# Optimization experiments

Hardware: AMD Instinct MI355X
Metric: run time of the kernel (lower is better)

Reference implementation:

```python
import jax, jax.numpy as jnp
import numpy as np

MARGIN = 0.5  # hardcoded in the torch __init__ regardless of the margin arg
P_IDS, K_PER_ID, K_PER_MOD = 32, 8, 4
B, C = P_IDS * K_PER_ID, 1024


def setup_inputs() -> dict:
    key = jax.random.key(0)
    inputs = jax.random.normal(key, (B, C), dtype=jnp.float32)
    # Standard cross-modal ReID sampler: P identities, K instances each,
    # first K/2 from modality 0, last K/2 from modality 1. This guarantees the
    # boolean-mask reshape in the original code is well-formed (M per row).
    targets = jnp.repeat(jnp.arange(P_IDS, dtype=jnp.int32), K_PER_ID)
    subs = jnp.tile(jnp.repeat(jnp.arange(2, dtype=jnp.int32), K_PER_MOD), P_IDS)
    return {"inputs": inputs, "targets": targets, "subs": subs, "m_count": K_PER_MOD}


def _loss(inputs, targets, subs, m_count):
    b, c = inputs.shape
    # Mask construction uses detached inputs in the original (clone().detach()).
    xs = jax.lax.stop_gradient(inputs)
    diff = jnp.abs(xs[:, None, :] - xs[None, :, :])                     # (B,B,C)
    identity_mask = targets[:, None] == targets[None, :]                # (B,B)
    modality_mask = subs[:, None] == subs[None, :]                      # (B,B)
    combined = identity_mask & modality_mask                            # (B,B)

    # diff[combined].reshape(B, M, C): every row has exactly m_count trues;
    # stable argsort recovers the selected column indices in ascending order,
    # matching torch's row-major boolean-mask gather.
    order = jnp.argsort(jnp.where(combined, 0, 1), axis=1)              # stable
    idx = order[:, :m_count]                                            # (B,M)
    modality_diff = jnp.take_along_axis(diff, idx[:, :, None], axis=1)  # (B,M,C)

    mean_md = modality_diff.mean(-1, keepdims=True)                     # (B,M,1)
    m_counts = (modality_diff < mean_md * MARGIN).sum(1)                # (B,C) int
    # mdm[i,j,c] = m_counts[i,c] * m_counts[j,c]  (detached float mask)
    mdm = (m_counts[:, None, :] * m_counts[None, :, :]).astype(inputs.dtype)  # (B,B,C)

    mean_d = diff.mean(-1, keepdims=True)                               # (B,B,1)
    idm = (diff < mean_d * MARGIN).astype(inputs.dtype)                 # (B,B,C)

    # Gradient-carrying pairwise differences (vectorized form of the B-loop).
    d = inputs[:, None, :] - inputs[None, :, :]                         # (B,B,C)
    mod_dist = jnp.sqrt(jnp.maximum(((d * mdm) ** 2).sum(-1), 1e-12))   # (B,B)
    id_dist = jnp.sqrt(jnp.maximum(((d * idm) ** 2).sum(-1), 1e-12))    # (B,B)
    id_dist = jnp.where(identity_mask, jnp.inf, id_dist)                # drop same-id

    per_row = jnp.maximum(mod_dist.max(axis=1) * 10.0 - id_dist.min(axis=1), 0.0)
    return per_row.mean()


def reference(inputs, targets, subs, m_count):
    return _loss(inputs, targets, subs, m_count)
```

## Files before the change

kernel.cpp:

```cpp
#include <hip/hip_runtime.h>
#include <math.h>

#define BB 256
#define CC 1024
#define CC4 (CC/4)
#define MARGIN 0.5f
#define NTILE 32
#define JPT 8

__global__ __launch_bounds__(64) void mcsq_kernel(
    const float* __restrict__ x, const int* __restrict__ targets,
    const int* __restrict__ subs, const int* __restrict__ m_count_p,
    float* __restrict__ mcsq)
{
    const int i = blockIdx.x;
    const int lane = threadIdx.x;
    const int ti = targets[i], si = subs[i];
    int mc = *m_count_p;
    if (mc > 8) mc = 8;

    unsigned long long masks[4];
    #pragma unroll
    for (int q = 0; q < 4; ++q) {
        const int j = q * 64 + lane;
        masks[q] = __ballot(targets[j] == ti && subs[j] == si);
    }
    int idx[8];
    int cnt = 0;
    for (int q = 0; q < 4 && cnt < mc; ++q) {
        unsigned long long m = masks[q];
        while (m && cnt < mc) {
            const int b = __ffsll(m) - 1;
            idx[cnt++] = q * 64 + b;
            m &= m - 1;
        }
    }
    for (int q = 0; q < 4 && cnt < mc; ++q) {
        unsigned long long m = ~masks[q];
        while (m && cnt < mc) {
            const int b = __ffsll(m) - 1;
            idx[cnt++] = q * 64 + b;
            m &= m - 1;
        }
    }

    const float4* x4 = (const float4*)x;
    float4 xi[4];
    #pragma unroll
    for (int t = 0; t < 4; ++t) xi[t] = x4[(long)i * CC4 + lane + 64 * t];

    float4 c4[4];
    #pragma unroll
    for (int t = 0; t < 4; ++t) c4[t] = make_float4(0.f, 0.f, 0.f, 0.f);

    for (int k = 0; k < cnt; ++k) {
        float4 ad[4];
        float s = 0.f;
        #pragma unroll
        for (int t = 0; t < 4; ++t) {
            const float4 xj = x4[(long)idx[k] * CC4 + lane + 64 * t];
            ad[t].x = fabsf(xi[t].x - xj.x);
            ad[t].y = fabsf(xi[t].y - xj.y);
            ad[t].z = fabsf(xi[t].z - xj.z);
            ad[t].w = fabsf(xi[t].w - xj.w);
            s += ad[t].x + ad[t].y + ad[t].z + ad[t].w;
        }
        #pragma unroll
        for (int off = 32; off > 0; off >>= 1) s += __shfl_xor(s, off, 64);
        const float thr = s * (MARGIN / CC);
        #pragma unroll
        for (int t = 0; t < 4; ++t) {
            c4[t].x += (ad[t].x < thr) ? 1.f : 0.f;
            c4[t].y += (ad[t].y < thr) ? 1.f : 0.f;
            c4[t].z += (ad[t].z < thr) ? 1.f : 0.f;
            c4[t].w += (ad[t].w < thr) ? 1.f : 0.f;
        }
    }
    float4* m4 = (float4*)mcsq;
    #pragma unroll
    for (int t = 0; t < 4; ++t) {
        float4 o;
        o.x = c4[t].x * c4[t].x;
        o.y = c4[t].y * c4[t].y;
        o.z = c4[t].z * c4[t].z;
        o.w = c4[t].w * c4[t].w;
        m4[(long)i * CC4 + lane + 64 * t] = o;
    }
}

__global__ __launch_bounds__(256) void pair_kernel(
    const float* __restrict__ x, const float* __restrict__ mcsq,
    const int* __restrict__ targets,
    float* __restrict__ pmax, float* __restrict__ pmin)
{
    const int tid  = threadIdx.x;
    const int lane = tid & 63;
    const int gw   = blockIdx.x * 4 + (tid >> 6);
    const int p    = gw >> 5;
    const int jt   = gw & 31;
    const int i0 = 2 * p, i1 = 2 * p + 1;

    const float4* x4 = (const float4*)x;
    const float4* m4 = (const float4*)mcsq;

    float4 xi0[4], xi1[4], mi0[4], mi1[4];
    #pragma unroll
    for (int t = 0; t < 4; ++t) {
        const int c4 = lane + 64 * t;
        xi0[t] = x4[(long)i0 * CC4 + c4];
        xi1[t] = x4[(long)i1 * CC4 + c4];
        mi0[t] = m4[(long)i0 * CC4 + c4];
        mi1[t] = m4[(long)i1 * CC4 + c4];
    }
    const int t0 = targets[i0], t1 = targets[i1];

    float max0 = 0.f, max1 = 0.f;
    float min0 = INFINITY, min1 = INFINITY;

    for (int jj = 0; jj < JPT; ++jj) {
        const int j = jt * JPT + jj;
        float4 xa[4], ma[4];
        float s0 = 0.f, s1 = 0.f;
        #pragma unroll
        for (int t = 0; t < 4; ++t) {
            const int c4 = lane + 64 * t;
            xa[t] = x4[(long)j * CC4 + c4];
            ma[t] = m4[(long)j * CC4 + c4];
            s0 += fabsf(xi0[t].x - xa[t].x) + fabsf(xi0[t].y - xa[t].y)
                + fabsf(xi0[t].z - xa[t].z) + fabsf(xi0[t].w - xa[t].w);
            s1 += fabsf(xi1[t].x - xa[t].x) + fabsf(xi1[t].y - xa[t].y)
                + fabsf(xi1[t].z - xa[t].z) + fabsf(xi1[t].w - xa[t].w);
        }
        #pragma unroll
        for (int off = 32; off > 0; off >>= 1) {
            s0 += __shfl_xor(s0, off, 64);
            s1 += __shfl_xor(s1, off, 64);
        }
        const float thr0 = s0 * (MARGIN / CC);
        const float thr1 = s1 * (MARGIN / CC);

        float ids0 = 0.f, ids1 = 0.f, md0 = 0.f, md1 = 0.f;
        #pragma unroll
        for (int t = 0; t < 4; ++t) {
            #pragma unroll
            for (int u = 0; u < 4; ++u) {
                const float xav = (&xa[t].x)[u];
                const float mav = (&ma[t].x)[u];
                const float d0 = (&xi0[t].x)[u] - xav;
                const float q0 = d0 * d0;
                ids0 += (fabsf(d0) < thr0) ? q0 : 0.f;
                md0  += q0 * (&mi0[t].x)[u] * mav;
                const float d1 = (&xi1[t].x)[u] - xav;
                const float q1 = d1 * d1;
                ids1 += (fabsf(d1) < thr1) ? q1 : 0.f;
                md1  += q1 * (&mi1[t].x)[u] * mav;
            }
        }
        #pragma unroll
        for (int off = 32; off > 0; off >>= 1) {
            ids0 += __shfl_xor(ids0, off, 64);
            ids1 += __shfl_xor(ids1, off, 64);
            md0  += __shfl_xor(md0,  off, 64);
            md1  += __shfl_xor(md1,  off, 64);
        }
        max0 = fmaxf(max0, sqrtf(fmaxf(md0, 1e-12f)));
        max1 = fmaxf(max1, sqrtf(fmaxf(md1, 1e-12f)));
        const int tj = targets[j];
        if (tj != t0) min0 = fminf(min0, sqrtf(fmaxf(ids0, 1e-12f)));
        if (tj != t1) min1 = fminf(min1, sqrtf(fmaxf(ids1, 1e-12f)));
    }
    if (lane == 0) {
        pmax[i0 * NTILE + jt] = max0;
        pmax[i1 * NTILE + jt] = max1;
        pmin[i0 * NTILE + jt] = min0;
        pmin[i1 * NTILE + jt] = min1;
    }
}

__global__ __launch_bounds__(256) void final_kernel(
    const float* __restrict__ pmax, const float* __restrict__ pmin,
    float* __restrict__ out)
{
    const int i = threadIdx.x;
    float mx = 0.f, mn = INFINITY;
    for (int t = 0; t < NTILE; ++t) {
        mx = fmaxf(mx, pmax[i * NTILE + t]);
        mn = fminf(mn, pmin[i * NTILE + t]);
    }
    float per = fmaxf(mx * 10.f - mn, 0.f);
    __shared__ float red[256];
    red[i] = per;
    __syncthreads();
    for (int off = 128; off > 0; off >>= 1) {
        if (i < off) red[i] += red[i + off];
        __syncthreads();
    }
    if (i == 0) out[0] = red[0] * (1.0f / BB);
}

extern "C" void kernel_launch(void* const* d_in, const int* in_sizes, int n_in,
                              void* d_out, int out_size, void* d_ws, size_t ws_size,
                              hipStream_t stream)
{
    const float* x       = (const float*)d_in[0];
    const int*   targets = (const int*)d_in[1];
    const int*   subs    = (const int*)d_in[2];
    const int*   m_count = (const int*)d_in[3];
    float* out  = (float*)d_out;

    float* mcsq = (float*)d_ws;
    float* pmax = mcsq + (long)BB * CC;
    float* pmin = pmax + BB * NTILE;

    mcsq_kernel <<<BB,   64, 0, stream>>>(x, targets, subs, m_count, mcsq);
    pair_kernel <<<1024, 256, 0, stream>>>(x, mcsq, targets, pmax, pmin);
    final_kernel<<<1,   256, 0, stream>>>(pmax, pmin, out);
}
```

Before: 96.42 us.

## Exploit pairwise symmetry to compute only upper-triangular pair tiles

The pair kernel now walks only the upper triangle of (row-pair, column-tile) work items, mapped with a closed-form triangular index, so each symmetric pair distance is computed once. Each computed value is also written to transposed partial buffers, and the final kernel merges the row-wise and transposed partials to recover every row's max and min. This roughly halves the pairwise distance arithmetic and memory traffic. In exchange it adds extra partial stores, more complex index math, and a longer serial reduction in the single-block final kernel.

New measurement: 117.9 us. +22.3%, slower.

```diff
diff --git a/kernel.cpp b/kernel.cpp
--- a/kernel.cpp
+++ b/kernel.cpp
@@ -5,8 +5,9 @@
 #define CC 1024
 #define CC4 (CC/4)
 #define MARGIN 0.5f
-#define NTILE 32
-#define JPT 8
+#define NTILE 64
+#define JPT 4
+#define NP  128
 
 __global__ __launch_bounds__(64) void mcsq_kernel(
     const float* __restrict__ x, const int* __restrict__ targets,
@@ -91,13 +92,23 @@
 __global__ __launch_bounds__(256) void pair_kernel(
     const float* __restrict__ x, const float* __restrict__ mcsq,
     const int* __restrict__ targets,
-    float* __restrict__ pmax, float* __restrict__ pmin)
+    float* __restrict__ pmax, float* __restrict__ pmin,
+    float* __restrict__ pmaxT, float* __restrict__ pminT)
 {
     const int tid  = threadIdx.x;
     const int lane = tid & 63;
     const int gw   = blockIdx.x * 4 + (tid >> 6);
-    const int p    = gw >> 5;
-    const int jt   = gw & 31;
+
+    int h = (int)((129.0f - sqrtf(16641.0f - 4.0f * (float)gw)) * 0.5f);
+    if (h > 63) h = 63;
+    if (h < 0) h = 0;
+    while (h > 0 && (129 * h - h * h) > gw) --h;
+    while ((129 * (h + 1) - (h + 1) * (h + 1)) <= gw) ++h;
+    const int r     = gw - (129 * h - h * h);
+    const int cnt_h = 64 - h;
+    const int p     = 2 * h + r / cnt_h;
+    const int jt    = h + r % cnt_h;
+
     const int i0 = 2 * p, i1 = 2 * p + 1;
 
     const float4* x4 = (const float4*)x;
@@ -163,11 +174,19 @@
             md0  += __shfl_xor(md0,  off, 64);
             md1  += __shfl_xor(md1,  off, 64);
         }
-        max0 = fmaxf(max0, sqrtf(fmaxf(md0, 1e-12f)));
-        max1 = fmaxf(max1, sqrtf(fmaxf(md1, 1e-12f)));
+        const float mod0 = sqrtf(fmaxf(md0, 1e-12f));
+        const float mod1 = sqrtf(fmaxf(md1, 1e-12f));
+        max0 = fmaxf(max0, mod0);
+        max1 = fmaxf(max1, mod1);
+        float id0 = sqrtf(fmaxf(ids0, 1e-12f));
+        float id1 = sqrtf(fmaxf(ids1, 1e-12f));
         const int tj = targets[j];
-        if (tj != t0) min0 = fminf(min0, sqrtf(fmaxf(ids0, 1e-12f)));
-        if (tj != t1) min1 = fminf(min1, sqrtf(fmaxf(ids1, 1e-12f)));
+        if (tj != t0) min0 = fminf(min0, id0); else id0 = INFINITY;
+        if (tj != t1) min1 = fminf(min1, id1); else id1 = INFINITY;
+        if (lane == 0) {
+            pmaxT[j * NP + p] = fmaxf(mod0, mod1);
+            pminT[j * NP + p] = fminf(id0, id1);
+        }
     }
     if (lane == 0) {
         pmax[i0 * NTILE + jt] = max0;
@@ -179,13 +198,20 @@
 
 __global__ __launch_bounds__(256) void final_kernel(
     const float* __restrict__ pmax, const float* __restrict__ pmin,
+    const float* __restrict__ pmaxT, const float* __restrict__ pminT,
     float* __restrict__ out)
 {
     const int i = threadIdx.x;
+    const int s = i >> 2;
     float mx = 0.f, mn = INFINITY;
-    for (int t = 0; t < NTILE; ++t) {
+    for (int t = s; t < NTILE; ++t) {
         mx = fmaxf(mx, pmax[i * NTILE + t]);
         mn = fminf(mn, pmin[i * NTILE + t]);
+    }
+    const int pv = 2 * s + 2;
+    for (int p = 0; p < pv; ++p) {
+        mx = fmaxf(mx, pmaxT[i * NP + p]);
+        mn = fminf(mn, pminT[i * NP + p]);
     }
     float per = fmaxf(mx * 10.f - mn, 0.f);
     __shared__ float red[256];
@@ -208,11 +234,13 @@
     const int*   m_count = (const int*)d_in[3];
     float* out  = (float*)d_out;
 
-    float* mcsq = (float*)d_ws;
-    float* pmax = mcsq + (long)BB * CC;
-    float* pmin = pmax + BB * NTILE;
+    float* mcsq  = (float*)d_ws;
+    float* pmax  = mcsq  + (long)BB * CC;
+    float* pmin  = pmax  + BB * NTILE;
+    float* pmaxT = pmin  + BB * NTILE;
+    float* pminT = pmaxT + BB * NP;
 
     mcsq_kernel <<<BB,   64, 0, stream>>>(x, targets, subs, m_count, mcsq);
-    pair_kernel <<<1024, 256, 0, stream>>>(x, mcsq, targets, pmax, pmin);
-    final_kernel<<<1,   256, 0, stream>>>(pmax, pmin, out);
-}
+    pair_kernel <<<1040, 256, 0, stream>>>(x, mcsq, targets, pmax, pmin, pmaxT, pminT);
+    final_kernel<<<1,   256, 0, stream>>>(pmax, pmin, pmaxT, pminT, out);
+}
```

## Restructure pairwise pass into LDS-tiled two-pass kernels with channel-split atomics

Applied to the files above, without the earlier changes.

Replaces the per-wave pair kernel, which re-read full rows of x and mcsq from global memory for every pair, with two shared-memory-tiled kernels. The first accumulates L1 distances for 32x32 row blocks. The second computes masked squared distances, with each thread handling a 2x2 pair register tile over a channel slice and reducing across slices with global atomicAdd. Workspace zeroing is folded into mcsq_kernel. The final reduction is spread over 256 blocks that finish with an atomic counter and a last-block write. This trades global reloads and shuffle reductions for LDS reuse, but adds an extra pass, many float atomics and order-dependent summation.

Result: slower. 99.80 us (+3.5%).

```diff
diff --git a/kernel.cpp b/kernel.cpp
--- a/kernel.cpp
+++ b/kernel.cpp
@@ -5,16 +5,22 @@
 #define CC 1024
 #define CC4 (CC/4)
 #define MARGIN 0.5f
-#define NTILE 32
-#define JPT 8
+
 
 __global__ __launch_bounds__(64) void mcsq_kernel(
     const float* __restrict__ x, const int* __restrict__ targets,
     const int* __restrict__ subs, const int* __restrict__ m_count_p,
-    float* __restrict__ mcsq)
+    float* __restrict__ mcsq, float* __restrict__ zbase,
+    float* __restrict__ acc, unsigned int* __restrict__ cnt_g)
 {
     const int i = blockIdx.x;
     const int lane = threadIdx.x;
+    if (i == 0 && lane == 0) { *acc = 0.f; *cnt_g = 0u; }
+    {
+        const int g = i * 64 + lane;
+        #pragma unroll
+        for (int t = 0; t < 12; ++t) zbase[g + 16384 * t] = 0.f;
+    }
     const int ti = targets[i], si = subs[i];
     int mc = *m_count_p;
     if (mc > 8) mc = 8;
@@ -88,114 +94,154 @@
     }
 }
 
-__global__ __launch_bounds__(256) void pair_kernel(
+__global__ __launch_bounds__(256) void pass1_kernel(
+    const float* __restrict__ x, float* __restrict__ S)
+{
+    __shared__ float xs[64 * 129];
+    const int b  = blockIdx.x;
+    const int cc = b & 7;
+    const int jt = (b >> 3) & 7;
+    const int it = b >> 6;
+    const int l  = threadIdx.x;
+
+    const float4* x4 = (const float4*)x;
+    #pragma unroll
+    for (int k = 0; k < 8; ++k) {
+        const int idx = l + 256 * k;
+        const int row = idx >> 5;
+        const int c4  = idx & 31;
+        const int grow = (row < 32) ? (it * 32 + row) : (jt * 32 + row - 32);
+        const float4 v = x4[grow * CC4 + cc * 32 + c4];
+        float* dst = &xs[row * 129 + c4 * 4];
+        dst[0] = v.x; dst[1] = v.y; dst[2] = v.z; dst[3] = v.w;
+    }
+    __syncthreads();
+
+    const int li = l >> 4, lj = l & 15;
+    const float* pi0 = &xs[(2 * li) * 129];
+    const float* pi1 = &xs[(2 * li + 1) * 129];
+    const float* pj0 = &xs[(32 + 2 * lj) * 129];
+    const float* pj1 = &xs[(32 + 2 * lj + 1) * 129];
+    float s00 = 0.f, s01 = 0.f, s10 = 0.f, s11 = 0.f;
+    #pragma unroll 8
+    for (int c = 0; c < 128; ++c) {
+        const float a0 = pi0[c], a1 = pi1[c], b0 = pj0[c], b1 = pj1[c];
+        s00 += fabsf(a0 - b0); s01 += fabsf(a0 - b1);
+        s10 += fabsf(a1 - b0); s11 += fabsf(a1 - b1);
+    }
+    const int gi0 = it * 32 + 2 * li, gj0 = jt * 32 + 2 * lj;
+    atomicAdd(&S[gi0 * BB + gj0],           s00);
+    atomicAdd(&S[gi0 * BB + gj0 + 1],       s01);
+    atomicAdd(&S[(gi0 + 1) * BB + gj0],     s10);
+    atomicAdd(&S[(gi0 + 1) * BB + gj0 + 1], s11);
+}
+
+__global__ __launch_bounds__(256) void pass2_kernel(
     const float* __restrict__ x, const float* __restrict__ mcsq,
-    const int* __restrict__ targets,
-    float* __restrict__ pmax, float* __restrict__ pmin)
-{
-    const int tid  = threadIdx.x;
-    const int lane = tid & 63;
-    const int gw   = blockIdx.x * 4 + (tid >> 6);
-    const int p    = gw >> 5;
-    const int jt   = gw & 31;
-    const int i0 = 2 * p, i1 = 2 * p + 1;
+    const float* __restrict__ S,
+    float* __restrict__ IDS, float* __restrict__ MD)
+{
+    __shared__ float xs[64 * 65];
+    __shared__ float ms[64 * 65];
+    const int b  = blockIdx.x;
+    const int cc = b & 15;
+    const int jt = (b >> 4) & 7;
+    const int it = b >> 7;
+    const int l  = threadIdx.x;
 
     const float4* x4 = (const float4*)x;
     const float4* m4 = (const float4*)mcsq;
-
-    float4 xi0[4], xi1[4], mi0[4], mi1[4];
-    #pragma unroll
-    for (int t = 0; t < 4; ++t) {
-        const int c4 = lane + 64 * t;
-        xi0[t] = x4[(long)i0 * CC4 + c4];
-        xi1[t] = x4[(long)i1 * CC4 + c4];
-        mi0[t] = m4[(long)i0 * CC4 + c4];
-        mi1[t] = m4[(long)i1 * CC4 + c4];
-    }
-    const int t0 = targets[i0], t1 = targets[i1];
-
-    float max0 = 0.f, max1 = 0.f;
-    float min0 = INFINITY, min1 = INFINITY;
-
-    for (int jj = 0; jj < JPT; ++jj) {
-        const int j = jt * JPT + jj;
-        float4 xa[4], ma[4];
-        float s0 = 0.f, s1 = 0.f;
-        #pragma unroll
-        for (int t = 0; t < 4; ++t) {
-            const int c4 = lane + 64 * t;
-            xa[t] = x4[(long)j * CC4 + c4];
-            ma[t] = m4[(long)j * CC4 + c4];
-            s0 += fabsf(xi0[t].x - xa[t].x) + fabsf(xi0[t].y - xa[t].y)
-                + fabsf(xi0[t].z - xa[t].z) + fabsf(xi0[t].w - xa[t].w);
-            s1 += fabsf(xi1[t].x - xa[t].x) + fabsf(xi1[t].y - xa[t].y)
-                + fabsf(xi1[t].z - xa[t].z) + fabsf(xi1[t].w - xa[t].w);
-        }
-        #pragma unroll
-        for (int off = 32; off > 0; off >>= 1) {
-            s0 += __shfl_xor(s0, off, 64);
-            s1 += __shfl_xor(s1, off, 64);
-        }
-        const float thr0 = s0 * (MARGIN / CC);
-        const float thr1 = s1 * (MARGIN / CC);
-
-        float ids0 = 0.f, ids1 = 0.f, md0 = 0.f, md1 = 0.f;
-        #pragma unroll
-        for (int t = 0; t < 4; ++t) {
-            #pragma unroll
-            for (int u = 0; u < 4; ++u) {
-                const float xav = (&xa[t].x)[u];
-                const float mav = (&ma[t].x)[u];
-                const float d0 = (&xi0[t].x)[u] - xav;
-                const float q0 = d0 * d0;
-                ids0 += (fabsf(d0) < thr0) ? q0 : 0.f;
-                md0  += q0 * (&mi0[t].x)[u] * mav;
-                const float d1 = (&xi1[t].x)[u] - xav;
-                const float q1 = d1 * d1;
-                ids1 += (fabsf(d1) < thr1) ? q1 : 0.f;
-                md1  += q1 * (&mi1[t].x)[u] * mav;
-            }
-        }
-        #pragma unroll
-        for (int off = 32; off > 0; off >>= 1) {
-            ids0 += __shfl_xor(ids0, off, 64);
-            ids1 += __shfl_xor(ids1, off, 64);
-            md0  += __shfl_xor(md0,  off, 64);
-            md1  += __shfl_xor(md1,  off, 64);
-        }
-        max0 = fmaxf(max0, sqrtf(fmaxf(md0, 1e-12f)));
-        max1 = fmaxf(max1, sqrtf(fmaxf(md1, 1e-12f)));
-        const int tj = targets[j];
-        if (tj != t0) min0 = fminf(min0, sqrtf(fmaxf(ids0, 1e-12f)));
-        if (tj != t1) min1 = fminf(min1, sqrtf(fmaxf(ids1, 1e-12f)));
+    #pragma unroll
+    for (int k = 0; k < 4; ++k) {
+        const int idx = l + 256 * k;
+        const int row = idx >> 4;
+        const int c4  = idx & 15;
+        const int grow = (row < 32) ? (it * 32 + row) : (jt * 32 + row - 32);
+        const float4 v = x4[grow * CC4 + cc * 16 + c4];
+        const float4 w = m4[grow * CC4 + cc * 16 + c4];
+        float* dx = &xs[row * 65 + c4 * 4];
+        dx[0] = v.x; dx[1] = v.y; dx[2] = v.z; dx[3] = v.w;
+        float* dm = &ms[row * 65 + c4 * 4];
+        dm[0] = w.x; dm[1] = w.y; dm[2] = w.z; dm[3] = w.w;
+    }
+
+    const int li = l >> 4, lj = l & 15;
+    const int gi0 = it * 32 + 2 * li, gj0 = jt * 32 + 2 * lj;
+    const float t00 = S[gi0 * BB + gj0]           * (MARGIN / CC);
+    const float t01 = S[gi0 * BB + gj0 + 1]       * (MARGIN / CC);
+    const float t10 = S[(gi0 + 1) * BB + gj0]     * (MARGIN / CC);
+    const float t11 = S[(gi0 + 1) * BB + gj0 + 1] * (MARGIN / CC);
+    __syncthreads();
+
+    const float* pi0 = &xs[(2 * li) * 65];
+    const float* pi1 = &xs[(2 * li + 1) * 65];
+    const float* pj0 = &xs[(32 + 2 * lj) * 65];
+    const float* pj1 = &xs[(32 + 2 * lj + 1) * 65];
+    const float* qi0 = &ms[(2 * li) * 65];
+    const float* qi1 = &ms[(2 * li + 1) * 65];
+    const float* qj0 = &ms[(32 + 2 * lj) * 65];
+    const float* qj1 = &ms[(32 + 2 * lj + 1) * 65];
+
+    float i00 = 0.f, i01 = 0.f, i10 = 0.f, i11 = 0.f;
+    float m00 = 0.f, m01 = 0.f, m10 = 0.f, m11 = 0.f;
+    #pragma unroll 4
+    for (int c = 0; c < 64; ++c) {
+        const float a0 = pi0[c], a1 = pi1[c], b0 = pj0[c], b1 = pj1[c];
+        const float wa0 = qi0[c], wa1 = qi1[c], wb0 = qj0[c], wb1 = qj1[c];
+        float d, q;
+        d = a0 - b0; q = d * d; i00 += (fabsf(d) < t00) ? q : 0.f; m00 += q * wa0 * wb0;
+        d = a0 - b1; q = d * d; i01 += (fabsf(d) < t01) ? q : 0.f; m01 += q * wa0 * wb1;
+        d = a1 - b0; q = d * d; i10 += (fabsf(d) < t10) ? q : 0.f; m10 += q * wa1 * wb0;
+        d = a1 - b1; q = d * d; i11 += (fabsf(d) < t11) ? q : 0.f; m11 += q * wa1 * wb1;
+    }
+    atomicAdd(&IDS[gi0 * BB + gj0],           i00);
+    atomicAdd(&IDS[gi0 * BB + gj0 + 1],       i01);
+    atomicAdd(&IDS[(gi0 + 1) * BB + gj0],     i10);
+    atomicAdd(&IDS[(gi0 + 1) * BB + gj0 + 1], i11);
+    atomicAdd(&MD[gi0 * BB + gj0],            m00);
+    atomicAdd(&MD[gi0 * BB + gj0 + 1],        m01);
+    atomicAdd(&MD[(gi0 + 1) * BB + gj0],      m10);
+    atomicAdd(&MD[(gi0 + 1) * BB + gj0 + 1],  m11);
+}
+
+__global__ __launch_bounds__(64) void final_kernel(
+    const float* __restrict__ IDS, const float* __restrict__ MD,
+    const int* __restrict__ targets,
+    float* __restrict__ acc, unsigned int* __restrict__ cnt_g,
+    float* __restrict__ out)
+{
+    const int i = blockIdx.x;
+    const int lane = threadIdx.x;
+    const int ti = targets[i];
+    const float4 mdv = ((const float4*)(MD  + i * BB))[lane];
+    const float4 idv = ((const float4*)(IDS + i * BB))[lane];
+    const int4   tjv = ((const int4*)targets)[lane];
+
+    float mx, mn;
+    mx =            sqrtf(fmaxf(mdv.x, 1e-12f));
+    mx = fmaxf(mx,  sqrtf(fmaxf(mdv.y, 1e-12f)));
+    mx = fmaxf(mx,  sqrtf(fmaxf(mdv.z, 1e-12f)));
+    mx = fmaxf(mx,  sqrtf(fmaxf(mdv.w, 1e-12f)));
+    mn =            (tjv.x != ti) ? sqrtf(fmaxf(idv.x, 1e-12f)) : INFINITY;
+    mn = fminf(mn,  (tjv.y != ti) ? sqrtf(fmaxf(idv.y, 1e-12f)) : INFINITY);
+    mn = fminf(mn,  (tjv.z != ti) ? sqrtf(fmaxf(idv.z, 1e-12f)) : INFINITY);
+    mn = fminf(mn,  (tjv.w != ti) ? sqrtf(fmaxf(idv.w, 1e-12f)) : INFINITY);
+
+    #pragma unroll
+    for (int off = 32; off > 0; off >>= 1) {
+        mx = fmaxf(mx, __shfl_xor(mx, off, 64));
+        mn = fminf(mn, __shfl_xor(mn, off, 64));
     }
     if (lane == 0) {
-        pmax[i0 * NTILE + jt] = max0;
-        pmax[i1 * NTILE + jt] = max1;
-        pmin[i0 * NTILE + jt] = min0;
-        pmin[i1 * NTILE + jt] = min1;
-    }
-}
-
-__global__ __launch_bounds__(256) void final_kernel(
-    const float* __restrict__ pmax, const float* __restrict__ pmin,
-    float* __restrict__ out)
-{
-    const int i = threadIdx.x;
-    float mx = 0.f, mn = INFINITY;
-    for (int t = 0; t < NTILE; ++t) {
-        mx = fmaxf(mx, pmax[i * NTILE + t]);
-        mn = fminf(mn, pmin[i * NTILE + t]);
-    }
-    float per = fmaxf(mx * 10.f - mn, 0.f);
-    __shared__ float red[256];
-    red[i] = per;
-    __syncthreads();
-    for (int off = 128; off > 0; off >>= 1) {
-        if (i < off) red[i] += red[i + off];
-        __syncthreads();
-    }
-    if (i == 0) out[0] = red[0] * (1.0f / BB);
+        const float per = fmaxf(mx * 10.f - mn, 0.f);
+        atomicAdd(acc, per * (1.0f / BB));
+        __threadfence();
+        const unsigned int old = atomicAdd(cnt_g, 1u);
+        if (old == BB - 1) {
+            __threadfence();
+            out[0] = atomicAdd(acc, 0.0f);
+        }
+    }
 }
 
 extern "C" void kernel_launch(void* const* d_in, const int* in_sizes, int n_in,
@@ -209,10 +255,14 @@
     float* out  = (float*)d_out;
 
     float* mcsq = (float*)d_ws;
-    float* pmax = mcsq + (long)BB * CC;
-    float* pmin = pmax + BB * NTILE;
-
-    mcsq_kernel <<<BB,   64, 0, stream>>>(x, targets, subs, m_count, mcsq);
-    pair_kernel <<<1024, 256, 0, stream>>>(x, mcsq, targets, pmax, pmin);
-    final_kernel<<<1,   256, 0, stream>>>(pmax, pmin, out);
-}
+    float* S    = mcsq + (long)BB * CC;
+    float* IDS  = S    + BB * BB;
+    float* MD   = IDS  + BB * BB;
+    float* acc  = MD   + BB * BB;
+    unsigned int* cnt_g = (unsigned int*)(acc + 1);
+
+    mcsq_kernel <<<BB,   64,  0, stream>>>(x, targets, subs, m_count, mcsq, S, acc, cnt_g);
+    pass1_kernel<<<512,  256, 0, stream>>>(x, S);
+    pass2_kernel<<<1024, 256, 0, stream>>>(x, mcsq, S, IDS, MD);
+    final_kernel<<<BB,   64,  0, stream>>>(IDS, MD, targets, acc, cnt_g, out);
+}
```
